# Kernel tuning notes

Hardware: AMD Instinct MI355X
Metric: run time of the kernel (lower is better)

Reference implementation:

```python
import jax, jax.numpy as jnp
import numpy as np

T, B, IN, H = 512, 4096, 1, 12

def setup_inputs() -> dict:
    key = jax.random.key(0)
    ks = jax.random.split(key, 7)
    s = 1.0 / np.sqrt(H)
    return {
        "X": jax.random.normal(ks[0], (T, B, IN), dtype=jnp.float32),
        "W_ih": jax.random.uniform(ks[1], (4 * H, IN), minval=-s, maxval=s, dtype=jnp.float32),
        "W_hh": jax.random.uniform(ks[2], (4 * H, H), minval=-s, maxval=s, dtype=jnp.float32),
        "b_ih": jax.random.uniform(ks[3], (4 * H,), minval=-s, maxval=s, dtype=jnp.float32),
        "b_hh": jax.random.uniform(ks[4], (4 * H,), minval=-s, maxval=s, dtype=jnp.float32),
        "fc_w": jax.random.uniform(ks[5], (1, H), minval=-s, maxval=s, dtype=jnp.float32),
        "fc_b": jax.random.uniform(ks[6], (1,), minval=-s, maxval=s, dtype=jnp.float32),
    }

def reference(X, W_ih, W_hh, b_ih, b_hh, fc_w, fc_b):
    # Precompute input contribution for all timesteps: [T, B, 4H]
    x_proj = jnp.einsum('tbi,gi->tbg', X, W_ih) + b_ih + b_hh
    h0 = jnp.zeros((X.shape[1], H), dtype=X.dtype)
    c0 = jnp.zeros_like(h0)

    def step(carry, xp_t):
        h, c = carry
        gates = xp_t + h @ W_hh.T  # [B, 4H]
        i, f, g, o = jnp.split(gates, 4, axis=-1)  # PyTorch gate order i,f,g,o
        i = jax.nn.sigmoid(i)
        f = jax.nn.sigmoid(f)
        g = jnp.tanh(g)
        o = jax.nn.sigmoid(o)
        c_new = f * c + i * g
        h_new = o * jnp.tanh(c_new)
        return (h_new, c_new), h_new

    _, hs = jax.lax.scan(step, (h0, c0), x_proj)  # hs: [T, B, H]
    return jnp.einsum('tbh,oh->tbo', hs, fc_w) + fc_b  # [T, B, 1]
```

## Files before the change

kernel.cpp:

```cpp
#include <hip/hip_runtime.h>


#define TT    512
#define NB    4096
#define HH    12
#define RPW   4
#define CHUNK 64
#define XPAD  68

typedef float v2f __attribute__((ext_vector_type(2)));

static __device__ __forceinline__ v2f pkfma(v2f a, v2f b, v2f c) {
#if __has_builtin(__builtin_elementwise_fma)
    return __builtin_elementwise_fma(a, b, c);
#else
    v2f r; r.x = fmaf(a.x, b.x, c.x); r.y = fmaf(a.y, b.y, c.y); return r;
#endif
}

#define SNEG   (-1.44269504088896340736f)
#define SPOS   ( 2.88539008177792681472f)
#define M2SPOS (-5.77078016355585362944f)

#define ROR(r) (0x120 + (r))

__global__ __launch_bounds__(64, 1)
void lstm_fused(const float* __restrict__ X,
                const float* __restrict__ W_ih,
                const float* __restrict__ W_hh,
                const float* __restrict__ b_ih,
                const float* __restrict__ b_hh,
                const float* __restrict__ fc_w,
                const float* __restrict__ fc_b,
                float* __restrict__ out)
{
    __shared__ float xchunk[RPW][XPAD];

    const int lane = threadIdx.x;
    const int row  = lane >> 4;
    const int j    = lane & 15;
    const int cellbase = blockIdx.x * RPW;
    const int cell = cellbase + row;

    int sid[16];
    sid[0] = j;
#define PROBE(r) sid[r] = __builtin_amdgcn_update_dpp(0, j, ROR(r), 0xF, 0xF, true);
    PROBE(1)  PROBE(2)  PROBE(3)  PROBE(4)  PROBE(5)
    PROBE(6)  PROBE(7)  PROBE(8)  PROBE(9)  PROBE(10)
    PROBE(11) PROBE(12) PROBE(13) PROBE(14) PROBE(15)
#undef PROBE

    const int jc = (j < HH) ? j : (HH - 1);
    v2f wifU[16], wgoU[16];
    #pragma unroll
    for (int r = 0; r < 16; ++r) {
        const int  s  = sid[r];
        const int  sc = (s < HH) ? s : (HH - 1);
        const float g = ((j >= HH) || (s < HH)) ? 1.0f : 0.0f;
        wifU[r].x = g * SNEG * W_hh[(0 * HH + jc) * HH + sc];
        wifU[r].y = g * SNEG * W_hh[(1 * HH + jc) * HH + sc];
        wgoU[r].x = g * SPOS * W_hh[(2 * HH + jc) * HH + sc];
        wgoU[r].y = g * SNEG * W_hh[(3 * HH + jc) * HH + sc];
    }
    v2f bif, bgo, wxif, wxgo;
    bif.x  = SNEG * (b_ih[0 * HH + jc] + b_hh[0 * HH + jc]);
    bif.y  = SNEG * (b_ih[1 * HH + jc] + b_hh[1 * HH + jc]);
    bgo.x  = SPOS * (b_ih[2 * HH + jc] + b_hh[2 * HH + jc]);
    bgo.y  = SNEG * (b_ih[3 * HH + jc] + b_hh[3 * HH + jc]);
    wxif.x = SNEG * W_ih[0 * HH + jc];
    wxif.y = SNEG * W_ih[1 * HH + jc];
    wxgo.x = SPOS * W_ih[2 * HH + jc];
    wxgo.y = SNEG * W_ih[3 * HH + jc];
    const float fcb  = fc_b[0];
    const float fcwj = (j < HH) ? fc_w[j] : 0.0f;

    float c2 = 0.0f;
    float hn = 0.0f;
    int hbits = 0;

    float pPend = 0.0f;
    unsigned offPrev = 0;
    float* const outp = out + cell;

    float4 gq = *(const float4*)(X + (size_t)lane * NB + cellbase);

    for (int tc = 0; tc < TT; tc += CHUNK) {
        xchunk[0][lane] = gq.x;
        xchunk[1][lane] = gq.y;
        xchunk[2][lane] = gq.z;
        xchunk[3][lane] = gq.w;
        if (tc + CHUNK < TT)
            gq = *(const float4*)(X + (size_t)(tc + CHUNK + lane) * NB + cellbase);

        float4 xq_next = *(const float4*)&xchunk[row][0];

        for (int t4 = 0; t4 < CHUNK; t4 += 4) {
            const float4 xq = xq_next;
            const int nx = (t4 + 4 < CHUNK) ? (t4 + 4) : t4;
            xq_next = *(const float4*)&xchunk[row][nx];
            const float xs[4] = {xq.x, xq.y, xq.z, xq.w};

            #pragma unroll
            for (int u = 0; u < 4; ++u) {
                v2f xvv; xvv.x = xs[u]; xvv.y = xs[u];
                v2f gifA = pkfma(xvv, wxif, bif);
                v2f goA  = pkfma(xvv, wxgo, bgo);
                v2f gifB; gifB.x = 0.0f; gifB.y = 0.0f;
                v2f goB;  goB.x  = 0.0f; goB.y  = 0.0f;
                {
                    v2f hk; hk.x = hn; hk.y = hn;
                    gifA = pkfma(wifU[0], hk, gifA);
                    goA  = pkfma(wgoU[0], hk, goA);
                }
#define XR(r) { \
                const int hr_##r = __builtin_amdgcn_update_dpp(0, hbits, ROR(r), 0xF, 0xF, true); \
                const float hf = __int_as_float(hr_##r); \
                v2f hk; hk.x = hf; hk.y = hf; \
                if ((r) < 8) { gifA = pkfma(wifU[r], hk, gifA); goA = pkfma(wgoU[r], hk, goA); } \
                else         { gifB = pkfma(wifU[r], hk, gifB); goB = pkfma(wgoU[r], hk, goB); } }
                XR(1)  XR(2)  XR(3)  XR(4)  XR(5)
                XR(6)  XR(7)  XR(8)  XR(9)  XR(10)
                XR(11) XR(12) XR(13) XR(14) XR(15)
#undef XR
                const v2f gif = gifA + gifB;
                const v2f ggo = goA + goB;

                const float Ei = __builtin_amdgcn_exp2f(gif.x);
                const float Ef = __builtin_amdgcn_exp2f(gif.y);
                const float Eg = __builtin_amdgcn_exp2f(ggo.x);
                const float Eo = __builtin_amdgcn_exp2f(ggo.y);

                float p = pPend;
                p += __int_as_float(__builtin_amdgcn_update_dpp(0, __float_as_int(p), ROR(8), 0xF, 0xF, true));
                p += __int_as_float(__builtin_amdgcn_update_dpp(0, __float_as_int(p), ROR(4), 0xF, 0xF, true));

                const float si = __builtin_amdgcn_rcpf(1.0f + Ei);
                const float sf = __builtin_amdgcn_rcpf(1.0f + Ef);
                const float rg = __builtin_amdgcn_rcpf(1.0f + Eg);
                const float so = __builtin_amdgcn_rcpf(1.0f + Eo);

                const float tgS = fmaf(M2SPOS, rg, SPOS);
                c2 = fmaf(sf, c2, si * tgS);
                const float Ec = __builtin_amdgcn_exp2f(c2);

                p += __int_as_float(__builtin_amdgcn_update_dpp(0, __float_as_int(p), ROR(2), 0xF, 0xF, true));
                p += __int_as_float(__builtin_amdgcn_update_dpp(0, __float_as_int(p), ROR(1), 0xF, 0xF, true));
                if (j == 0) *(float*)((char*)outp + offPrev) = p + fcb;

                const float rc   = __builtin_amdgcn_rcpf(1.0f + Ec);
                const float m2so = -2.0f * so;
                hn    = fmaf(m2so, rc, so);
                hbits = __float_as_int(hn);

                pPend   = hn * fcwj;
                offPrev = (unsigned)(tc + t4 + u) << 14;
            }
        }
    }

    {
        float p = pPend;
        p += __int_as_float(__builtin_amdgcn_update_dpp(0, __float_as_int(p), ROR(8), 0xF, 0xF, true));
        p += __int_as_float(__builtin_amdgcn_update_dpp(0, __float_as_int(p), ROR(4), 0xF, 0xF, true));
        p += __int_as_float(__builtin_amdgcn_update_dpp(0, __float_as_int(p), ROR(2), 0xF, 0xF, true));
        p += __int_as_float(__builtin_amdgcn_update_dpp(0, __float_as_int(p), ROR(1), 0xF, 0xF, true));
        if (j == 0) *(float*)((char*)outp + offPrev) = p + fcb;
    }
}

extern "C" void kernel_launch(void* const* d_in, const int* in_sizes, int n_in,
                              void* d_out, int out_size, void* d_ws, size_t ws_size,
                              hipStream_t stream) {
    const float* X    = (const float*)d_in[0];
    const float* W_ih = (const float*)d_in[1];
    const float* W_hh = (const float*)d_in[2];
    const float* b_ih = (const float*)d_in[3];
    const float* b_hh = (const float*)d_in[4];
    const float* fc_w = (const float*)d_in[5];
    const float* fc_b = (const float*)d_in[6];
    float* out = (float*)d_out;

    const int grid = NB / RPW;
    lstm_fused<<<grid, 64, 0, stream>>>(X, W_ih, W_hh, b_ih, b_hh, fc_w, fc_b, out);
}
```

Measured before the change: 182.2 us.

## Exchange hidden state through LDS instead of DPP row rotations

Each step, every lane writes its new hidden value to a per-row shared-memory buffer. After a wave barrier, all lanes read the full 12-element h vector back with vector loads. Gate FMAs then run over contiguous weight pairs instead of 15 DPP-rotated broadcasts, and the FC output projection is computed directly from the shared h vector, removing the DPP reduction tree. This trades DPP cross-lane latency for an LDS write/read round-trip on the serial recurrence path.

```diff
diff --git a/kernel.cpp b/kernel.cpp
--- a/kernel.cpp
+++ b/kernel.cpp
@@ -7,8 +7,10 @@
 #define RPW   4
 #define CHUNK 64
 #define XPAD  68
+#define HSTR  20
 
 typedef float v2f __attribute__((ext_vector_type(2)));
+typedef float v4f __attribute__((ext_vector_type(4)));
 
 static __device__ __forceinline__ v2f pkfma(v2f a, v2f b, v2f c) {
 #if __has_builtin(__builtin_elementwise_fma)
@@ -21,8 +23,6 @@
 #define SNEG   (-1.44269504088896340736f)
 #define SPOS   ( 2.88539008177792681472f)
 #define M2SPOS (-5.77078016355585362944f)
-
-#define ROR(r) (0x120 + (r))
 
 __global__ __launch_bounds__(64, 1)
 void lstm_fused(const float* __restrict__ X,
@@ -34,7 +34,8 @@
                 const float* __restrict__ fc_b,
                 float* __restrict__ out)
 {
-    __shared__ float xchunk[RPW][XPAD];
+    __shared__ __align__(16) float xchunk[RPW][XPAD];
+    __shared__ __align__(16) float hsh[RPW][HSTR];
 
     const int lane = threadIdx.x;
     const int row  = lane >> 4;
@@ -42,45 +43,43 @@
     const int cellbase = blockIdx.x * RPW;
     const int cell = cellbase + row;
 
-    int sid[16];
-    sid[0] = j;
-#define PROBE(r) sid[r] = __builtin_amdgcn_update_dpp(0, j, ROR(r), 0xF, 0xF, true);
-    PROBE(1)  PROBE(2)  PROBE(3)  PROBE(4)  PROBE(5)
-    PROBE(6)  PROBE(7)  PROBE(8)  PROBE(9)  PROBE(10)
-    PROBE(11) PROBE(12) PROBE(13) PROBE(14) PROBE(15)
-#undef PROBE
-
     const int jc = (j < HH) ? j : (HH - 1);
-    v2f wifU[16], wgoU[16];
+
+    v2f wI[6], wF[6], wG[6], wO[6], fcv[6];
     #pragma unroll
-    for (int r = 0; r < 16; ++r) {
-        const int  s  = sid[r];
-        const int  sc = (s < HH) ? s : (HH - 1);
-        const float g = ((j >= HH) || (s < HH)) ? 1.0f : 0.0f;
-        wifU[r].x = g * SNEG * W_hh[(0 * HH + jc) * HH + sc];
-        wifU[r].y = g * SNEG * W_hh[(1 * HH + jc) * HH + sc];
-        wgoU[r].x = g * SPOS * W_hh[(2 * HH + jc) * HH + sc];
-        wgoU[r].y = g * SNEG * W_hh[(3 * HH + jc) * HH + sc];
+    for (int k = 0; k < 6; ++k) {
+        const float* r0 = W_hh + (0 * HH + jc) * HH + 2 * k;
+        const float* r1 = W_hh + (1 * HH + jc) * HH + 2 * k;
+        const float* r2 = W_hh + (2 * HH + jc) * HH + 2 * k;
+        const float* r3 = W_hh + (3 * HH + jc) * HH + 2 * k;
+        wI[k].x = SNEG * r0[0];  wI[k].y = SNEG * r0[1];
+        wF[k].x = SNEG * r1[0];  wF[k].y = SNEG * r1[1];
+        wG[k].x = SPOS * r2[0];  wG[k].y = SPOS * r2[1];
+        wO[k].x = SNEG * r3[0];  wO[k].y = SNEG * r3[1];
+        fcv[k].x = fc_w[2 * k];  fcv[k].y = fc_w[2 * k + 1];
     }
-    v2f bif, bgo, wxif, wxgo;
-    bif.x  = SNEG * (b_ih[0 * HH + jc] + b_hh[0 * HH + jc]);
-    bif.y  = SNEG * (b_ih[1 * HH + jc] + b_hh[1 * HH + jc]);
-    bgo.x  = SPOS * (b_ih[2 * HH + jc] + b_hh[2 * HH + jc]);
-    bgo.y  = SNEG * (b_ih[3 * HH + jc] + b_hh[3 * HH + jc]);
-    wxif.x = SNEG * W_ih[0 * HH + jc];
-    wxif.y = SNEG * W_ih[1 * HH + jc];
-    wxgo.x = SPOS * W_ih[2 * HH + jc];
-    wxgo.y = SNEG * W_ih[3 * HH + jc];
-    const float fcb  = fc_b[0];
-    const float fcwj = (j < HH) ? fc_w[j] : 0.0f;
+    v2f wxI, wxF, wxG, wxO, bI, bF, bG, bO, bFC;
+    wxI.x = SNEG * W_ih[0 * HH + jc];  wxI.y = 0.0f;
+    wxF.x = SNEG * W_ih[1 * HH + jc];  wxF.y = 0.0f;
+    wxG.x = SPOS * W_ih[2 * HH + jc];  wxG.y = 0.0f;
+    wxO.x = SNEG * W_ih[3 * HH + jc];  wxO.y = 0.0f;
+    bI.x = SNEG * (b_ih[0 * HH + jc] + b_hh[0 * HH + jc]);  bI.y = 0.0f;
+    bF.x = SNEG * (b_ih[1 * HH + jc] + b_hh[1 * HH + jc]);  bF.y = 0.0f;
+    bG.x = SPOS * (b_ih[2 * HH + jc] + b_hh[2 * HH + jc]);  bG.y = 0.0f;
+    bO.x = SNEG * (b_ih[3 * HH + jc] + b_hh[3 * HH + jc]);  bO.y = 0.0f;
+    bFC.x = fc_b[0];  bFC.y = 0.0f;
 
     float c2 = 0.0f;
     float hn = 0.0f;
-    int hbits = 0;
-
-    float pPend = 0.0f;
+
+    float* const hrow = &hsh[row][0];
+    const int wslot = j;
+
     unsigned offPrev = 0;
     float* const outp = out + cell;
+
+    hrow[wslot] = 0.0f;
+    __builtin_amdgcn_wave_barrier();
 
     float4 gq = *(const float4*)(X + (size_t)lane * NB + cellbase);
 
@@ -102,37 +101,52 @@
 
             #pragma unroll
             for (int u = 0; u < 4; ++u) {
+                const v4f ha = *(const v4f*)&hrow[0];
+                const v4f hb = *(const v4f*)&hrow[4];
+                const v4f hc = *(const v4f*)&hrow[8];
+                v2f hp0; hp0.x = ha.x; hp0.y = ha.y;
+                v2f hp1; hp1.x = ha.z; hp1.y = ha.w;
+                v2f hp2; hp2.x = hb.x; hp2.y = hb.y;
+                v2f hp3; hp3.x = hb.z; hp3.y = hb.w;
+                v2f hp4; hp4.x = hc.x; hp4.y = hc.y;
+                v2f hp5; hp5.x = hc.z; hp5.y = hc.w;
+
                 v2f xvv; xvv.x = xs[u]; xvv.y = xs[u];
-                v2f gifA = pkfma(xvv, wxif, bif);
-                v2f goA  = pkfma(xvv, wxgo, bgo);
-                v2f gifB; gifB.x = 0.0f; gifB.y = 0.0f;
-                v2f goB;  goB.x  = 0.0f; goB.y  = 0.0f;
-                {
-                    v2f hk; hk.x = hn; hk.y = hn;
-                    gifA = pkfma(wifU[0], hk, gifA);
-                    goA  = pkfma(wgoU[0], hk, goA);
-                }
-#define XR(r) { \
-                const int hr_##r = __builtin_amdgcn_update_dpp(0, hbits, ROR(r), 0xF, 0xF, true); \
-                const float hf = __int_as_float(hr_##r); \
-                v2f hk; hk.x = hf; hk.y = hf; \
-                if ((r) < 8) { gifA = pkfma(wifU[r], hk, gifA); goA = pkfma(wgoU[r], hk, goA); } \
-                else         { gifB = pkfma(wifU[r], hk, gifB); goB = pkfma(wgoU[r], hk, goB); } }
-                XR(1)  XR(2)  XR(3)  XR(4)  XR(5)
-                XR(6)  XR(7)  XR(8)  XR(9)  XR(10)
-                XR(11) XR(12) XR(13) XR(14) XR(15)
-#undef XR
-                const v2f gif = gifA + gifB;
-                const v2f ggo = goA + goB;
-
-                const float Ei = __builtin_amdgcn_exp2f(gif.x);
-                const float Ef = __builtin_amdgcn_exp2f(gif.y);
-                const float Eg = __builtin_amdgcn_exp2f(ggo.x);
-                const float Eo = __builtin_amdgcn_exp2f(ggo.y);
-
-                float p = pPend;
-                p += __int_as_float(__builtin_amdgcn_update_dpp(0, __float_as_int(p), ROR(8), 0xF, 0xF, true));
-                p += __int_as_float(__builtin_amdgcn_update_dpp(0, __float_as_int(p), ROR(4), 0xF, 0xF, true));
+                v2f aI = pkfma(xvv, wxI, bI);
+                v2f aF = pkfma(xvv, wxF, bF);
+                v2f aG = pkfma(xvv, wxG, bG);
+                v2f aO = pkfma(xvv, wxO, bO);
+                v2f pf = pkfma(fcv[0], hp0, bFC);
+                aI = pkfma(wI[0], hp0, aI);  aF = pkfma(wF[0], hp0, aF);
+                aG = pkfma(wG[0], hp0, aG);  aO = pkfma(wO[0], hp0, aO);
+                aI = pkfma(wI[1], hp1, aI);  aF = pkfma(wF[1], hp1, aF);
+                aG = pkfma(wG[1], hp1, aG);  aO = pkfma(wO[1], hp1, aO);
+                pf = pkfma(fcv[1], hp1, pf);
+                aI = pkfma(wI[2], hp2, aI);  aF = pkfma(wF[2], hp2, aF);
+                aG = pkfma(wG[2], hp2, aG);  aO = pkfma(wO[2], hp2, aO);
+                pf = pkfma(fcv[2], hp2, pf);
+                aI = pkfma(wI[3], hp3, aI);  aF = pkfma(wF[3], hp3, aF);
+                aG = pkfma(wG[3], hp3, aG);  aO = pkfma(wO[3], hp3, aO);
+                pf = pkfma(fcv[3], hp3, pf);
+                aI = pkfma(wI[4], hp4, aI);  aF = pkfma(wF[4], hp4, aF);
+                aG = pkfma(wG[4], hp4, aG);  aO = pkfma(wO[4], hp4, aO);
+                pf = pkfma(fcv[4], hp4, pf);
+                aI = pkfma(wI[5], hp5, aI);  aF = pkfma(wF[5], hp5, aF);
+                aG = pkfma(wG[5], hp5, aG);  aO = pkfma(wO[5], hp5, aO);
+                pf = pkfma(fcv[5], hp5, pf);
+
+                const float gi = aI.x + aI.y;
+                const float gf = aF.x + aF.y;
+                const float gg = aG.x + aG.y;
+                const float go = aO.x + aO.y;
+
+                const float Ei = __builtin_amdgcn_exp2f(gi);
+                const float Ef = __builtin_amdgcn_exp2f(gf);
+                const float Eg = __builtin_amdgcn_exp2f(gg);
+                const float Eo = __builtin_amdgcn_exp2f(go);
+
+                const float p = pf.x + pf.y;
+                if (j == 0) *(float*)((char*)outp + offPrev) = p;
 
                 const float si = __builtin_amdgcn_rcpf(1.0f + Ei);
                 const float sf = __builtin_amdgcn_rcpf(1.0f + Ef);
@@ -142,29 +156,36 @@
                 const float tgS = fmaf(M2SPOS, rg, SPOS);
                 c2 = fmaf(sf, c2, si * tgS);
                 const float Ec = __builtin_amdgcn_exp2f(c2);
-
-                p += __int_as_float(__builtin_amdgcn_update_dpp(0, __float_as_int(p), ROR(2), 0xF, 0xF, true));
-                p += __int_as_float(__builtin_amdgcn_update_dpp(0, __float_as_int(p), ROR(1), 0xF, 0xF, true));
-                if (j == 0) *(float*)((char*)outp + offPrev) = p + fcb;
-
-                const float rc   = __builtin_amdgcn_rcpf(1.0f + Ec);
+                const float rc = __builtin_amdgcn_rcpf(1.0f + Ec);
                 const float m2so = -2.0f * so;
-                hn    = fmaf(m2so, rc, so);
-                hbits = __float_as_int(hn);
-
-                pPend   = hn * fcwj;
+                hn = fmaf(m2so, rc, so);
+
+                hrow[wslot] = hn;
+                __builtin_amdgcn_wave_barrier();
+
                 offPrev = (unsigned)(tc + t4 + u) << 14;
             }
         }
     }
 
     {
-        float p = pPend;
-        p += __int_as_float(__builtin_amdgcn_update_dpp(0, __float_as_int(p), ROR(8), 0xF, 0xF, true));
-        p += __int_as_float(__builtin_amdgcn_update_dpp(0, __float_as_int(p), ROR(4), 0xF, 0xF, true));
-        p += __int_as_float(__builtin_amdgcn_update_dpp(0, __float_as_int(p), ROR(2), 0xF, 0xF, true));
-        p += __int_as_float(__builtin_amdgcn_update_dpp(0, __float_as_int(p), ROR(1), 0xF, 0xF, true));
-        if (j == 0) *(float*)((char*)outp + offPrev) = p + fcb;
+        const v4f ha = *(const v4f*)&hrow[0];
+        const v4f hb = *(const v4f*)&hrow[4];
+        const v4f hc = *(const v4f*)&hrow[8];
+        v2f hp0; hp0.x = ha.x; hp0.y = ha.y;
+        v2f hp1; hp1.x = ha.z; hp1.y = ha.w;
+        v2f hp2; hp2.x = hb.x; hp2.y = hb.y;
+        v2f hp3; hp3.x = hb.z; hp3.y = hb.w;
+        v2f hp4; hp4.x = hc.x; hp4.y = hc.y;
+        v2f hp5; hp5.x = hc.z; hp5.y = hc.w;
+        v2f pf = pkfma(fcv[0], hp0, bFC);
+        pf = pkfma(fcv[1], hp1, pf);
+        pf = pkfma(fcv[2], hp2, pf);
+        pf = pkfma(fcv[3], hp3, pf);
+        pf = pkfma(fcv[4], hp4, pf);
+        pf = pkfma(fcv[5], hp5, pf);
+        const float p = pf.x + pf.y;
+        if (j == 0) *(float*)((char*)outp + offPrev) = p;
     }
 }
 
```

Result: faster. 176.6 us, median of 2 (-3.1%).

## Split LSTM gates across two half-waves per cell with swizzle exchange

Applied to the files above, without the earlier changes.

Each 64-lane wave now handles 2 cells instead of 4, with the two 16-lane halves of each cell computing different gate pairs (i/f vs g/o). This halves the recurrent FMA and transcendental work per lane per timestep, and doubles the number of waves to improve latency hiding. Gate results and the new hidden state are exchanged between halves with ds_swizzle. These add cross-lane latency to the serial recurrence and increase total instruction count.

```diff
diff --git a/kernel.cpp b/kernel.cpp
--- a/kernel.cpp
+++ b/kernel.cpp
@@ -4,7 +4,7 @@
 #define TT    512
 #define NB    4096
 #define HH    12
-#define RPW   4
+#define RPW   2
 #define CHUNK 64
 #define XPAD  68
 
@@ -17,14 +17,20 @@
     v2f r; r.x = fmaf(a.x, b.x, c.x); r.y = fmaf(a.y, b.y, c.y); return r;
 #endif
 }
+static __device__ __forceinline__ v2f splat2(float s) { v2f r; r.x = s; r.y = s; return r; }
 
 #define SNEG   (-1.44269504088896340736f)
 #define SPOS   ( 2.88539008177792681472f)
 #define M2SPOS (-5.77078016355585362944f)
 
 #define ROR(r) (0x120 + (r))
+#define SWZ_XOR16 0x401F
 
-__global__ __launch_bounds__(64, 1)
+static __device__ __forceinline__ float swz16(float v) {
+    return __int_as_float(__builtin_amdgcn_ds_swizzle(__float_as_int(v), SWZ_XOR16));
+}
+
+__global__ __launch_bounds__(64, 2)
 void lstm_fused(const float* __restrict__ X,
                 const float* __restrict__ W_ih,
                 const float* __restrict__ W_hh,
@@ -34,13 +40,14 @@
                 const float* __restrict__ fc_b,
                 float* __restrict__ out)
 {
-    __shared__ float xchunk[RPW][XPAD];
+    __shared__ __align__(16) float xchunk[RPW][XPAD];
 
     const int lane = threadIdx.x;
-    const int row  = lane >> 4;
+    const int cell = lane >> 5;
+    const int half = (lane >> 4) & 1;
     const int j    = lane & 15;
     const int cellbase = blockIdx.x * RPW;
-    const int cell = cellbase + row;
+    const int gcell = cellbase + cell;
 
     int sid[16];
     sid[0] = j;
@@ -51,26 +58,27 @@
 #undef PROBE
 
     const int jc = (j < HH) ? j : (HH - 1);
-    v2f wifU[16], wgoU[16];
+
+    const int   gA = (half ? 2 : 0) * HH + jc;
+    const int   gB = (half ? 3 : 1) * HH + jc;
+    const float sA = half ? SPOS : SNEG;
+    const float* WA = W_hh + gA * HH;
+    const float* WB = W_hh + gB * HH;
+    v2f wU[16];
     #pragma unroll
     for (int r = 0; r < 16; ++r) {
         const int  s  = sid[r];
         const int  sc = (s < HH) ? s : (HH - 1);
         const float g = ((j >= HH) || (s < HH)) ? 1.0f : 0.0f;
-        wifU[r].x = g * SNEG * W_hh[(0 * HH + jc) * HH + sc];
-        wifU[r].y = g * SNEG * W_hh[(1 * HH + jc) * HH + sc];
-        wgoU[r].x = g * SPOS * W_hh[(2 * HH + jc) * HH + sc];
-        wgoU[r].y = g * SNEG * W_hh[(3 * HH + jc) * HH + sc];
+        wU[r].x = g * sA   * WA[sc];
+        wU[r].y = g * SNEG * WB[sc];
     }
-    v2f bif, bgo, wxif, wxgo;
-    bif.x  = SNEG * (b_ih[0 * HH + jc] + b_hh[0 * HH + jc]);
-    bif.y  = SNEG * (b_ih[1 * HH + jc] + b_hh[1 * HH + jc]);
-    bgo.x  = SPOS * (b_ih[2 * HH + jc] + b_hh[2 * HH + jc]);
-    bgo.y  = SNEG * (b_ih[3 * HH + jc] + b_hh[3 * HH + jc]);
-    wxif.x = SNEG * W_ih[0 * HH + jc];
-    wxif.y = SNEG * W_ih[1 * HH + jc];
-    wxgo.x = SPOS * W_ih[2 * HH + jc];
-    wxgo.y = SNEG * W_ih[3 * HH + jc];
+    v2f wxv, bv;
+    wxv.x = sA   * W_ih[gA];
+    wxv.y = SNEG * W_ih[gB];
+    bv.x  = sA   * (b_ih[gA] + b_hh[gA]);
+    bv.y  = SNEG * (b_ih[gB] + b_hh[gB]);
+
     const float fcb  = fc_b[0];
     const float fcwj = (j < HH) ? fc_w[j] : 0.0f;
 
@@ -80,76 +88,68 @@
 
     float pPend = 0.0f;
     unsigned offPrev = 0;
-    float* const outp = out + cell;
+    float* const outp = out + gcell;
 
-    float4 gq = *(const float4*)(X + (size_t)lane * NB + cellbase);
+    float2 gq = *(const float2*)(X + (size_t)lane * NB + cellbase);
 
     for (int tc = 0; tc < TT; tc += CHUNK) {
         xchunk[0][lane] = gq.x;
         xchunk[1][lane] = gq.y;
-        xchunk[2][lane] = gq.z;
-        xchunk[3][lane] = gq.w;
         if (tc + CHUNK < TT)
-            gq = *(const float4*)(X + (size_t)(tc + CHUNK + lane) * NB + cellbase);
+            gq = *(const float2*)(X + (size_t)(tc + CHUNK + lane) * NB + cellbase);
+        __builtin_amdgcn_wave_barrier();
 
-        float4 xq_next = *(const float4*)&xchunk[row][0];
+        float4 xq_next = *(const float4*)&xchunk[cell][0];
 
         for (int t4 = 0; t4 < CHUNK; t4 += 4) {
             const float4 xq = xq_next;
             const int nx = (t4 + 4 < CHUNK) ? (t4 + 4) : t4;
-            xq_next = *(const float4*)&xchunk[row][nx];
+            xq_next = *(const float4*)&xchunk[cell][nx];
             const float xs[4] = {xq.x, xq.y, xq.z, xq.w};
 
             #pragma unroll
             for (int u = 0; u < 4; ++u) {
-                v2f xvv; xvv.x = xs[u]; xvv.y = xs[u];
-                v2f gifA = pkfma(xvv, wxif, bif);
-                v2f goA  = pkfma(xvv, wxgo, bgo);
-                v2f gifB; gifB.x = 0.0f; gifB.y = 0.0f;
-                v2f goB;  goB.x  = 0.0f; goB.y  = 0.0f;
-                {
-                    v2f hk; hk.x = hn; hk.y = hn;
-                    gifA = pkfma(wifU[0], hk, gifA);
-                    goA  = pkfma(wgoU[0], hk, goA);
-                }
+                v2f aA = pkfma(splat2(xs[u]), wxv, bv);
+                v2f aB; aB.x = 0.0f; aB.y = 0.0f;
+                aA = pkfma(wU[0], splat2(hn), aA);
 #define XR(r) { \
                 const int hr_##r = __builtin_amdgcn_update_dpp(0, hbits, ROR(r), 0xF, 0xF, true); \
-                const float hf = __int_as_float(hr_##r); \
-                v2f hk; hk.x = hf; hk.y = hf; \
-                if ((r) < 8) { gifA = pkfma(wifU[r], hk, gifA); goA = pkfma(wgoU[r], hk, goA); } \
-                else         { gifB = pkfma(wifU[r], hk, gifB); goB = pkfma(wgoU[r], hk, goB); } }
+                const v2f hk = splat2(__int_as_float(hr_##r)); \
+                if ((r) < 8) { aA = pkfma(wU[r], hk, aA); } \
+                else         { aB = pkfma(wU[r], hk, aB); } }
                 XR(1)  XR(2)  XR(3)  XR(4)  XR(5)
                 XR(6)  XR(7)  XR(8)  XR(9)  XR(10)
                 XR(11) XR(12) XR(13) XR(14) XR(15)
 #undef XR
-                const v2f gif = gifA + gifB;
-                const v2f ggo = goA + goB;
+                const v2f a = aA + aB;
 
-                const float Ei = __builtin_amdgcn_exp2f(gif.x);
-                const float Ef = __builtin_amdgcn_exp2f(gif.y);
-                const float Eg = __builtin_amdgcn_exp2f(ggo.x);
-                const float Eo = __builtin_amdgcn_exp2f(ggo.y);
+                const float E0 = __builtin_amdgcn_exp2f(a.x);
+                const float E1 = __builtin_amdgcn_exp2f(a.y);
 
                 float p = pPend;
                 p += __int_as_float(__builtin_amdgcn_update_dpp(0, __float_as_int(p), ROR(8), 0xF, 0xF, true));
                 p += __int_as_float(__builtin_amdgcn_update_dpp(0, __float_as_int(p), ROR(4), 0xF, 0xF, true));
 
-                const float si = __builtin_amdgcn_rcpf(1.0f + Ei);
-                const float sf = __builtin_amdgcn_rcpf(1.0f + Ef);
-                const float rg = __builtin_amdgcn_rcpf(1.0f + Eg);
-                const float so = __builtin_amdgcn_rcpf(1.0f + Eo);
+                const float r0 = __builtin_amdgcn_rcpf(1.0f + E0);
+                const float r1 = __builtin_amdgcn_rcpf(1.0f + E1);
+                const float t0 = fmaf(M2SPOS, r0, SPOS);
 
-                const float tgS = fmaf(M2SPOS, rg, SPOS);
-                c2 = fmaf(sf, c2, si * tgS);
+                const float x0 = swz16(t0);
+                const float x1 = swz16(r1);
+
+                c2 = fmaf(r1, c2, r0 * x0);
                 const float Ec = __builtin_amdgcn_exp2f(c2);
 
                 p += __int_as_float(__builtin_amdgcn_update_dpp(0, __float_as_int(p), ROR(2), 0xF, 0xF, true));
                 p += __int_as_float(__builtin_amdgcn_update_dpp(0, __float_as_int(p), ROR(1), 0xF, 0xF, true));
-                if (j == 0) *(float*)((char*)outp + offPrev) = p + fcb;
+                if (j == 0 && half == 0) *(float*)((char*)outp + offPrev) = p + fcb;
 
-                const float rc   = __builtin_amdgcn_rcpf(1.0f + Ec);
-                const float m2so = -2.0f * so;
-                hn    = fmaf(m2so, rc, so);
+                const float rc = __builtin_amdgcn_rcpf(1.0f + Ec);
+                const float m2 = -2.0f * x1;
+                hn = fmaf(m2, rc, x1);
+
+                const float ph = swz16(hn);
+                hn = (half == 0) ? hn : ph;
                 hbits = __float_as_int(hn);
 
                 pPend   = hn * fcwj;
@@ -164,7 +164,7 @@
         p += __int_as_float(__builtin_amdgcn_update_dpp(0, __float_as_int(p), ROR(4), 0xF, 0xF, true));
         p += __int_as_float(__builtin_amdgcn_update_dpp(0, __float_as_int(p), ROR(2), 0xF, 0xF, true));
         p += __int_as_float(__builtin_amdgcn_update_dpp(0, __float_as_int(p), ROR(1), 0xF, 0xF, true));
-        if (j == 0) *(float*)((char*)outp + offPrev) = p + fcb;
+        if (j == 0 && half == 0) *(float*)((char*)outp + offPrev) = p + fcb;
     }
 }
 
```

Result: slower. 216.2 us (+18.6%).

## Pack recurrent matvec by neighbor pairs, fuse FC head, share sigmoid reciprocals

Applied to the files above, without the earlier changes.

The packed FMAs now pair two neighbor h values per gate instead of pairing two gates per h value. Each gate gets two split accumulators that are reduced horizontally at the end. The FC output is computed from the already-gathered neighbor h values, which removes the separate DPP reduction chain for the output. Sigmoids are computed two at a time with one reciprocal of a product, cutting transcendental ops but adding multiplies and some risk of overflow or precision loss when both exponentials are large.

```diff
diff --git a/kernel.cpp b/kernel.cpp
--- a/kernel.cpp
+++ b/kernel.cpp
@@ -34,7 +34,7 @@
                 const float* __restrict__ fc_b,
                 float* __restrict__ out)
 {
-    __shared__ float xchunk[RPW][XPAD];
+    __shared__ __align__(16) float xchunk[RPW][XPAD];
 
     const int lane = threadIdx.x;
     const int row  = lane >> 4;
@@ -51,34 +51,40 @@
 #undef PROBE
 
     const int jc = (j < HH) ? j : (HH - 1);
-    v2f wifU[16], wgoU[16];
+
+    v2f wIp[8], wFp[8], wGp[8], wOp[8], fcP[8];
+    const float* Wi = W_hh + (0 * HH + jc) * HH;
+    const float* Wf = W_hh + (1 * HH + jc) * HH;
+    const float* Wg = W_hh + (2 * HH + jc) * HH;
+    const float* Wo = W_hh + (3 * HH + jc) * HH;
     #pragma unroll
-    for (int r = 0; r < 16; ++r) {
-        const int  s  = sid[r];
-        const int  sc = (s < HH) ? s : (HH - 1);
-        const float g = ((j >= HH) || (s < HH)) ? 1.0f : 0.0f;
-        wifU[r].x = g * SNEG * W_hh[(0 * HH + jc) * HH + sc];
-        wifU[r].y = g * SNEG * W_hh[(1 * HH + jc) * HH + sc];
-        wgoU[r].x = g * SPOS * W_hh[(2 * HH + jc) * HH + sc];
-        wgoU[r].y = g * SNEG * W_hh[(3 * HH + jc) * HH + sc];
+    for (int p = 0; p < 8; ++p) {
+        const int s0 = sid[2 * p], s1 = sid[2 * p + 1];
+        const int sc0 = (s0 < HH) ? s0 : (HH - 1);
+        const int sc1 = (s1 < HH) ? s1 : (HH - 1);
+        const float g0 = ((j >= HH) || (s0 < HH)) ? 1.0f : 0.0f;
+        const float g1 = ((j >= HH) || (s1 < HH)) ? 1.0f : 0.0f;
+        wIp[p].x = g0 * SNEG * Wi[sc0];  wIp[p].y = g1 * SNEG * Wi[sc1];
+        wFp[p].x = g0 * SNEG * Wf[sc0];  wFp[p].y = g1 * SNEG * Wf[sc1];
+        wGp[p].x = g0 * SPOS * Wg[sc0];  wGp[p].y = g1 * SPOS * Wg[sc1];
+        wOp[p].x = g0 * SNEG * Wo[sc0];  wOp[p].y = g1 * SNEG * Wo[sc1];
+        fcP[p].x = (s0 < HH) ? fc_w[s0] : 0.0f;
+        fcP[p].y = (s1 < HH) ? fc_w[s1] : 0.0f;
     }
-    v2f bif, bgo, wxif, wxgo;
-    bif.x  = SNEG * (b_ih[0 * HH + jc] + b_hh[0 * HH + jc]);
-    bif.y  = SNEG * (b_ih[1 * HH + jc] + b_hh[1 * HH + jc]);
-    bgo.x  = SPOS * (b_ih[2 * HH + jc] + b_hh[2 * HH + jc]);
-    bgo.y  = SNEG * (b_ih[3 * HH + jc] + b_hh[3 * HH + jc]);
-    wxif.x = SNEG * W_ih[0 * HH + jc];
-    wxif.y = SNEG * W_ih[1 * HH + jc];
-    wxgo.x = SPOS * W_ih[2 * HH + jc];
-    wxgo.y = SNEG * W_ih[3 * HH + jc];
-    const float fcb  = fc_b[0];
-    const float fcwj = (j < HH) ? fc_w[j] : 0.0f;
+    const float wxI = SNEG * W_ih[0 * HH + jc];
+    const float wxF = SNEG * W_ih[1 * HH + jc];
+    const float wxG = SPOS * W_ih[2 * HH + jc];
+    const float wxO = SNEG * W_ih[3 * HH + jc];
+    const float bI = SNEG * (b_ih[0 * HH + jc] + b_hh[0 * HH + jc]);
+    const float bF = SNEG * (b_ih[1 * HH + jc] + b_hh[1 * HH + jc]);
+    const float bG = SPOS * (b_ih[2 * HH + jc] + b_hh[2 * HH + jc]);
+    const float bO = SNEG * (b_ih[3 * HH + jc] + b_hh[3 * HH + jc]);
+    v2f bFCv; bFCv.x = fc_b[0]; bFCv.y = 0.0f;
 
     float c2 = 0.0f;
     float hn = 0.0f;
     int hbits = 0;
 
-    float pPend = 0.0f;
     unsigned offPrev = 0;
     float* const outp = out + cell;
 
@@ -102,69 +108,108 @@
 
             #pragma unroll
             for (int u = 0; u < 4; ++u) {
-                v2f xvv; xvv.x = xs[u]; xvv.y = xs[u];
-                v2f gifA = pkfma(xvv, wxif, bif);
-                v2f goA  = pkfma(xvv, wxgo, bgo);
-                v2f gifB; gifB.x = 0.0f; gifB.y = 0.0f;
-                v2f goB;  goB.x  = 0.0f; goB.y  = 0.0f;
-                {
-                    v2f hk; hk.x = hn; hk.y = hn;
-                    gifA = pkfma(wifU[0], hk, gifA);
-                    goA  = pkfma(wgoU[0], hk, goA);
+                v2f hp[8];
+                hp[0].x = hn;
+#define GR(r, dst) dst = __int_as_float(__builtin_amdgcn_update_dpp(0, hbits, ROR(r), 0xF, 0xF, true));
+                GR(1,  hp[0].y)
+                GR(2,  hp[1].x)  GR(3,  hp[1].y)
+                GR(4,  hp[2].x)  GR(5,  hp[2].y)
+                GR(6,  hp[3].x)  GR(7,  hp[3].y)
+                GR(8,  hp[4].x)  GR(9,  hp[4].y)
+                GR(10, hp[5].x)  GR(11, hp[5].y)
+                GR(12, hp[6].x)  GR(13, hp[6].y)
+                GR(14, hp[7].x)  GR(15, hp[7].y)
+#undef GR
+
+                v2f aI; aI.x = fmaf(xs[u], wxI, bI); aI.y = 0.0f;
+                v2f aF; aF.x = fmaf(xs[u], wxF, bF); aF.y = 0.0f;
+                v2f aG; aG.x = fmaf(xs[u], wxG, bG); aG.y = 0.0f;
+                v2f aO; aO.x = fmaf(xs[u], wxO, bO); aO.y = 0.0f;
+                v2f bIa; bIa.x = 0.0f; bIa.y = 0.0f;
+                v2f bFa = bIa, bGa = bIa, bOa = bIa;
+                #pragma unroll
+                for (int p = 0; p < 4; ++p) {
+                    aI  = pkfma(wIp[p],     hp[p],     aI);
+                    aF  = pkfma(wFp[p],     hp[p],     aF);
+                    aG  = pkfma(wGp[p],     hp[p],     aG);
+                    aO  = pkfma(wOp[p],     hp[p],     aO);
+                    bIa = pkfma(wIp[p + 4], hp[p + 4], bIa);
+                    bFa = pkfma(wFp[p + 4], hp[p + 4], bFa);
+                    bGa = pkfma(wGp[p + 4], hp[p + 4], bGa);
+                    bOa = pkfma(wOp[p + 4], hp[p + 4], bOa);
                 }
-#define XR(r) { \
-                const int hr_##r = __builtin_amdgcn_update_dpp(0, hbits, ROR(r), 0xF, 0xF, true); \
-                const float hf = __int_as_float(hr_##r); \
-                v2f hk; hk.x = hf; hk.y = hf; \
-                if ((r) < 8) { gifA = pkfma(wifU[r], hk, gifA); goA = pkfma(wgoU[r], hk, goA); } \
-                else         { gifB = pkfma(wifU[r], hk, gifB); goB = pkfma(wgoU[r], hk, goB); } }
-                XR(1)  XR(2)  XR(3)  XR(4)  XR(5)
-                XR(6)  XR(7)  XR(8)  XR(9)  XR(10)
-                XR(11) XR(12) XR(13) XR(14) XR(15)
-#undef XR
-                const v2f gif = gifA + gifB;
-                const v2f ggo = goA + goB;
-
-                const float Ei = __builtin_amdgcn_exp2f(gif.x);
-                const float Ef = __builtin_amdgcn_exp2f(gif.y);
-                const float Eg = __builtin_amdgcn_exp2f(ggo.x);
-                const float Eo = __builtin_amdgcn_exp2f(ggo.y);
-
-                float p = pPend;
-                p += __int_as_float(__builtin_amdgcn_update_dpp(0, __float_as_int(p), ROR(8), 0xF, 0xF, true));
-                p += __int_as_float(__builtin_amdgcn_update_dpp(0, __float_as_int(p), ROR(4), 0xF, 0xF, true));
-
-                const float si = __builtin_amdgcn_rcpf(1.0f + Ei);
-                const float sf = __builtin_amdgcn_rcpf(1.0f + Ef);
-                const float rg = __builtin_amdgcn_rcpf(1.0f + Eg);
-                const float so = __builtin_amdgcn_rcpf(1.0f + Eo);
+                const v2f sI = aI + bIa;
+                const v2f sF = aF + bFa;
+                const v2f sG = aG + bGa;
+                const v2f sO = aO + bOa;
+                const float gi = sI.x + sI.y;
+                const float gf = sF.x + sF.y;
+                const float gg = sG.x + sG.y;
+                const float go = sO.x + sO.y;
+
+                const float Ei = __builtin_amdgcn_exp2f(gi);
+                const float Ef = __builtin_amdgcn_exp2f(gf);
+                const float Eg = __builtin_amdgcn_exp2f(gg);
+                const float Eo = __builtin_amdgcn_exp2f(go);
+
+                v2f pf = pkfma(fcP[0], hp[0], bFCv);
+                pf = pkfma(fcP[1], hp[1], pf);
+                pf = pkfma(fcP[2], hp[2], pf);
+                pf = pkfma(fcP[3], hp[3], pf);
+                pf = pkfma(fcP[4], hp[4], pf);
+                pf = pkfma(fcP[5], hp[5], pf);
+                pf = pkfma(fcP[6], hp[6], pf);
+                pf = pkfma(fcP[7], hp[7], pf);
+                const float p = pf.x + pf.y;
+                if (j == 0) *(float*)((char*)outp + offPrev) = p;
+
+                const float pi = 1.0f + Ei;
+                const float pF = 1.0f + Ef;
+                const float pg = 1.0f + Eg;
+                const float po = 1.0f + Eo;
+                const float rif = __builtin_amdgcn_rcpf(pi * pF);
+                const float rgo = __builtin_amdgcn_rcpf(pg * po);
+                const float si = pF * rif;
+                const float sf = pi * rif;
+                const float rg = po * rgo;
+                const float so = pg * rgo;
 
                 const float tgS = fmaf(M2SPOS, rg, SPOS);
                 c2 = fmaf(sf, c2, si * tgS);
                 const float Ec = __builtin_amdgcn_exp2f(c2);
-
-                p += __int_as_float(__builtin_amdgcn_update_dpp(0, __float_as_int(p), ROR(2), 0xF, 0xF, true));
-                p += __int_as_float(__builtin_amdgcn_update_dpp(0, __float_as_int(p), ROR(1), 0xF, 0xF, true));
-                if (j == 0) *(float*)((char*)outp + offPrev) = p + fcb;
-
-                const float rc   = __builtin_amdgcn_rcpf(1.0f + Ec);
+                const float rc = __builtin_amdgcn_rcpf(1.0f + Ec);
                 const float m2so = -2.0f * so;
-                hn    = fmaf(m2so, rc, so);
+                hn = fmaf(m2so, rc, so);
                 hbits = __float_as_int(hn);
 
-                pPend   = hn * fcwj;
                 offPrev = (unsigned)(tc + t4 + u) << 14;
             }
         }
     }
 
     {
-        float p = pPend;
-        p += __int_as_float(__builtin_amdgcn_update_dpp(0, __float_as_int(p), ROR(8), 0xF, 0xF, true));
-        p += __int_as_float(__builtin_amdgcn_update_dpp(0, __float_as_int(p), ROR(4), 0xF, 0xF, true));
-        p += __int_as_float(__builtin_amdgcn_update_dpp(0, __float_as_int(p), ROR(2), 0xF, 0xF, true));
-        p += __int_as_float(__builtin_amdgcn_update_dpp(0, __float_as_int(p), ROR(1), 0xF, 0xF, true));
-        if (j == 0) *(float*)((char*)outp + offPrev) = p + fcb;
+        v2f hp[8];
+        hp[0].x = hn;
+#define GR(r, dst) dst = __int_as_float(__builtin_amdgcn_update_dpp(0, hbits, ROR(r), 0xF, 0xF, true));
+        GR(1,  hp[0].y)
+        GR(2,  hp[1].x)  GR(3,  hp[1].y)
+        GR(4,  hp[2].x)  GR(5,  hp[2].y)
+        GR(6,  hp[3].x)  GR(7,  hp[3].y)
+        GR(8,  hp[4].x)  GR(9,  hp[4].y)
+        GR(10, hp[5].x)  GR(11, hp[5].y)
+        GR(12, hp[6].x)  GR(13, hp[6].y)
+        GR(14, hp[7].x)  GR(15, hp[7].y)
+#undef GR
+        v2f pf = pkfma(fcP[0], hp[0], bFCv);
+        pf = pkfma(fcP[1], hp[1], pf);
+        pf = pkfma(fcP[2], hp[2], pf);
+        pf = pkfma(fcP[3], hp[3], pf);
+        pf = pkfma(fcP[4], hp[4], pf);
+        pf = pkfma(fcP[5], hp[5], pf);
+        pf = pkfma(fcP[6], hp[6], pf);
+        pf = pkfma(fcP[7], hp[7], pf);
+        const float p = pf.x + pf.y;
+        if (j == 0) *(float*)((char*)outp + offPrev) = p;
     }
 }
 
```

Measured after the change: 198.9 us. 1.09x slower.
